# Kernel tuning notes

Measured on AMD Instinct MI355X. Metric: run time of the kernel, lower is better.

Reference implementation:

```python
import jax, jax.numpy as jnp
import numpy as np

B, N, M, H = 32, 1024, 128, 2  # batch, memory slots, word size, read heads
EPS = 1e-8


def setup_inputs() -> dict:
    key = jax.random.key(0)
    ks = jax.random.split(key, 6)
    return {
        "read_keys": jax.random.normal(ks[0], (B, H, M), jnp.float32),
        "read_strengths": jax.random.uniform(ks[1], (B, H), jnp.float32),
        "read_mode": jax.random.uniform(ks[2], (B, H, 3), jnp.float32),
        "W_old": jax.random.uniform(ks[3], (B, N), jnp.float32),
        "L": jax.random.uniform(ks[4], (B, N, N), jnp.float32),
        "memory": jax.random.normal(ks[5], (B, N, M), jnp.float32),
        "head_no": 0,
    }


def reference(read_keys, read_strengths, read_mode, W_old, L, memory, head_no):
    # Select this head's parameters
    k = read_keys[:, head_no, :]                      # [B, M]
    beta = read_strengths[:, head_no][:, None]        # [B, 1]
    rm = read_mode[:, head_no, :]                     # [B, 3] (backward, content, forward)

    # Temporal link transitions: f = L @ w_old, b = L^T @ w_old
    f = jnp.einsum('bij,bj->bi', L, W_old)            # [B, N]
    b = jnp.einsum('bji,bj->bi', L, W_old)            # [B, N]

    # Content-based addressing: softmax(beta * cosine_similarity(k, memory))
    sim = jnp.einsum('bnm,bm->bn', memory, k)         # [B, N]
    denom = (jnp.linalg.norm(memory, axis=-1)
             * jnp.linalg.norm(k, axis=-1, keepdims=True)) + EPS
    C = jax.nn.softmax(beta * sim / denom, axis=-1)   # [B, N]

    # Read-mode weighted combination
    W = rm[:, 0:1] * b + rm[:, 1:2] * C + rm[:, 2:3] * f  # [B, N]

    # Memory read
    mem_content = jnp.einsum('bn,bnm->bm', W, memory)     # [B, M]
    return (W, mem_content)
```

## Files before the change

### kernel.cpp

```cpp
#include <hip/hip_runtime.h>
#include <math.h>

#define EPS 1e-8f

constexpr int B = 32, N = 1024, M = 128, H = 2;

constexpr int ROWS_A   = 32;
constexpr int CHUNKS_A = N / ROWS_A;
constexpr int ROWS_C2   = 64;
constexpr int CHUNKS_C2 = N / ROWS_C2;

__global__ __launch_bounds__(256) void kA(const float* __restrict__ L,
                                          const float* __restrict__ Wold,
                                          float* __restrict__ f,
                                          float* __restrict__ bpart) {
    int bid   = blockIdx.x;
    int b     = bid / CHUNKS_A;
    int chunk = bid % CHUNKS_A;
    int t     = threadIdx.x;
    int lane  = t & 63, wave = t >> 6;

    __shared__ float sw[N];
    __shared__ float lds_b[4][N];

    reinterpret_cast<float4*>(sw)[t] =
        reinterpret_cast<const float4*>(Wold + (size_t)b * N)[t];
    __syncthreads();

    float4 wreg[4];
    float4 bacc[4];
#pragma unroll
    for (int s = 0; s < 4; ++s) {
        wreg[s] = reinterpret_cast<float4*>(sw)[lane + 64 * s];
        bacc[s] = make_float4(0.f, 0.f, 0.f, 0.f);
    }

    const float* Lb = L + (size_t)b * N * N;
    int r0 = chunk * ROWS_A;
    for (int r = wave; r < ROWS_A; r += 4) {
        int i = r0 + r;
        const float4* row = reinterpret_cast<const float4*>(Lb + (size_t)i * N);
        float wi = sw[i];
        float p  = 0.f;
#pragma unroll
        for (int s = 0; s < 4; ++s) {
            float4 v = row[lane + 64 * s];
            p += v.x * wreg[s].x + v.y * wreg[s].y + v.z * wreg[s].z + v.w * wreg[s].w;
            bacc[s].x += v.x * wi;
            bacc[s].y += v.y * wi;
            bacc[s].z += v.z * wi;
            bacc[s].w += v.w * wi;
        }
#pragma unroll
        for (int off = 32; off; off >>= 1) p += __shfl_down(p, off, 64);
        if (lane == 0) f[(size_t)b * N + i] = p;
    }

#pragma unroll
    for (int s = 0; s < 4; ++s)
        reinterpret_cast<float4*>(lds_b[wave])[lane + 64 * s] = bacc[s];
    __syncthreads();

    float4 s0 = reinterpret_cast<float4*>(lds_b[0])[t];
    float4 s1 = reinterpret_cast<float4*>(lds_b[1])[t];
    float4 s2 = reinterpret_cast<float4*>(lds_b[2])[t];
    float4 s3 = reinterpret_cast<float4*>(lds_b[3])[t];
    float4 o;
    o.x = s0.x + s1.x + s2.x + s3.x;
    o.y = s0.y + s1.y + s2.y + s3.y;
    o.z = s0.z + s1.z + s2.z + s3.z;
    o.w = s0.w + s1.w + s2.w + s3.w;
    reinterpret_cast<float4*>(bpart + ((size_t)b * CHUNKS_A + chunk) * N)[t] = o;
}

__global__ __launch_bounds__(256) void kB(const float* __restrict__ mem,
                                          const float* __restrict__ keys,
                                          const float* __restrict__ strengths,
                                          const int* __restrict__ head,
                                          float* __restrict__ logits) {
    int h    = head[0];
    int bid  = blockIdx.x;
    int b    = bid / (N / 4);
    int c    = bid % (N / 4);
    int lane = threadIdx.x & 63, wave = threadIdx.x >> 6;
    int n    = c * 4 + wave;

    float2 kv = reinterpret_cast<const float2*>(keys + ((size_t)b * H + h) * M)[lane];
    float2 mv = reinterpret_cast<const float2*>(mem + ((size_t)b * N + n) * M)[lane];

    float dot = mv.x * kv.x + mv.y * kv.y;
    float sm  = mv.x * mv.x + mv.y * mv.y;
    float sk  = kv.x * kv.x + kv.y * kv.y;
#pragma unroll
    for (int off = 32; off; off >>= 1) {
        dot += __shfl_down(dot, off, 64);
        sm  += __shfl_down(sm, off, 64);
        sk  += __shfl_down(sk, off, 64);
    }
    if (lane == 0) {
        float beta  = strengths[(size_t)b * H + h];
        float denom = sqrtf(sm) * sqrtf(sk) + EPS;
        logits[(size_t)b * N + n] = beta * dot / denom;
    }
}

__global__ __launch_bounds__(256) void kC1(const float* __restrict__ f,
                                           const float* __restrict__ bpart,
                                           const float* __restrict__ logits,
                                           const float* __restrict__ mode,
                                           const int* __restrict__ head,
                                           float* __restrict__ Wout) {
    int b = blockIdx.x;
    int t = threadIdx.x;
    int h = head[0];
    int lane = t & 63, wave = t >> 6;
    __shared__ float redmax[4];
    __shared__ float redsum[4];

    float lg[4], bs[4], fv[4];
    float mx = -1e30f;
#pragma unroll
    for (int q = 0; q < 4; ++q) {
        int n = t + 256 * q;
        lg[q] = logits[(size_t)b * N + n];
        fv[q] = f[(size_t)b * N + n];
        float s = 0.f;
        for (int c = 0; c < CHUNKS_A; ++c)
            s += bpart[((size_t)b * CHUNKS_A + c) * N + n];
        bs[q] = s;
        mx = fmaxf(mx, lg[q]);
    }
#pragma unroll
    for (int off = 32; off; off >>= 1) mx = fmaxf(mx, __shfl_down(mx, off, 64));
    if (lane == 0) redmax[wave] = mx;
    __syncthreads();
    mx = fmaxf(fmaxf(redmax[0], redmax[1]), fmaxf(redmax[2], redmax[3]));

    float ex[4];
    float se = 0.f;
#pragma unroll
    for (int q = 0; q < 4; ++q) { ex[q] = expf(lg[q] - mx); se += ex[q]; }
#pragma unroll
    for (int off = 32; off; off >>= 1) se += __shfl_down(se, off, 64);
    if (lane == 0) redsum[wave] = se;
    __syncthreads();
    se = redsum[0] + redsum[1] + redsum[2] + redsum[3];
    float inv = 1.f / se;

    const float* rm = mode + ((size_t)b * H + h) * 3;
    float rm0 = rm[0], rm1 = rm[1], rm2 = rm[2];
#pragma unroll
    for (int q = 0; q < 4; ++q) {
        int n = t + 256 * q;
        Wout[(size_t)b * N + n] = rm0 * bs[q] + rm1 * ex[q] * inv + rm2 * fv[q];
    }
}

__global__ __launch_bounds__(256) void kC2(const float* __restrict__ mem,
                                           const float* __restrict__ Wout,
                                           float* __restrict__ mcpart) {
    int bid   = blockIdx.x;
    int b     = bid / CHUNKS_C2;
    int chunk = bid % CHUNKS_C2;
    int t     = threadIdx.x;
    int cg    = t & 31;
    int rg    = t >> 5;
    __shared__ float4 lds[8][32];

    float4 acc = make_float4(0.f, 0.f, 0.f, 0.f);
    int r0 = chunk * ROWS_C2;
#pragma unroll
    for (int rr = 0; rr < ROWS_C2 / 8; ++rr) {
        int n   = r0 + rg + rr * 8;
        float w = Wout[(size_t)b * N + n];
        float4 v = reinterpret_cast<const float4*>(mem + ((size_t)b * N + n) * M)[cg];
        acc.x += w * v.x; acc.y += w * v.y; acc.z += w * v.z; acc.w += w * v.w;
    }
    lds[rg][cg] = acc;
    __syncthreads();
    if (t < 32) {
        float4 o = make_float4(0.f, 0.f, 0.f, 0.f);
#pragma unroll
        for (int g = 0; g < 8; ++g) {
            float4 v = lds[g][t];
            o.x += v.x; o.y += v.y; o.z += v.z; o.w += v.w;
        }
        reinterpret_cast<float4*>(mcpart + ((size_t)b * CHUNKS_C2 + chunk) * M)[t] = o;
    }
}

__global__ __launch_bounds__(256) void kC3(const float* __restrict__ mcpart,
                                           float* __restrict__ mc) {
    int idx = blockIdx.x * 256 + threadIdx.x;
    if (idx >= B * M) return;
    int b = idx / M, m = idx % M;
    float s = 0.f;
    for (int c = 0; c < CHUNKS_C2; ++c)
        s += mcpart[((size_t)b * CHUNKS_C2 + c) * M + m];
    mc[idx] = s;
}

extern "C" void kernel_launch(void* const* d_in, const int* in_sizes, int n_in,
                              void* d_out, int out_size, void* d_ws, size_t ws_size,
                              hipStream_t stream) {
    const float* read_keys      = (const float*)d_in[0];
    const float* read_strengths = (const float*)d_in[1];
    const float* read_mode      = (const float*)d_in[2];
    const float* W_old          = (const float*)d_in[3];
    const float* L              = (const float*)d_in[4];
    const float* memory         = (const float*)d_in[5];
    const int*   head_no        = (const int*)d_in[6];

    float* out_W  = (float*)d_out;
    float* out_mc = out_W + (size_t)B * N;

    float* ws     = (float*)d_ws;
    float* f      = ws;
    float* bpart  = f + (size_t)B * N;
    float* logits = bpart + (size_t)B * CHUNKS_A * N;
    float* mcpart = logits + (size_t)B * N;

    kA<<<B * CHUNKS_A, 256, 0, stream>>>(L, W_old, f, bpart);
    kB<<<B * (N / 4), 256, 0, stream>>>(memory, read_keys, read_strengths, head_no, logits);
    kC1<<<B, 256, 0, stream>>>(f, bpart, logits, read_mode, head_no, out_W);
    kC2<<<B * CHUNKS_C2, 256, 0, stream>>>(memory, out_W, mcpart);
    kC3<<<(B * M + 255) / 256, 256, 0, stream>>>(mcpart, out_mc);
}
```

Before: 44.07 us.

## Merge link and content kernels, split W into linear parts, cut launches to three

```diff
diff --git a/kernel.cpp b/kernel.cpp
--- a/kernel.cpp
+++ b/kernel.cpp
@@ -5,199 +5,223 @@
 
 constexpr int B = 32, N = 1024, M = 128, H = 2;
 
-constexpr int ROWS_A   = 32;
+constexpr int ROWS_A   = 16;
 constexpr int CHUNKS_A = N / ROWS_A;
-constexpr int ROWS_C2   = 64;
-constexpr int CHUNKS_C2 = N / ROWS_C2;
-
-__global__ __launch_bounds__(256) void kA(const float* __restrict__ L,
+constexpr int NBLK_A   = B * CHUNKS_A;
+constexpr int ROWS_B   = 64;
+constexpr int NBLK_B   = B * (N / ROWS_B);
+constexpr int ROWS_C   = 64;
+constexpr int CHUNKS_C = N / ROWS_C;
+
+__global__ __launch_bounds__(256) void k1(const float* __restrict__ L,
                                           const float* __restrict__ Wold,
-                                          float* __restrict__ f,
-                                          float* __restrict__ bpart) {
-    int bid   = blockIdx.x;
-    int b     = bid / CHUNKS_A;
-    int chunk = bid % CHUNKS_A;
-    int t     = threadIdx.x;
-    int lane  = t & 63, wave = t >> 6;
-
-    __shared__ float sw[N];
-    __shared__ float lds_b[4][N];
-
-    reinterpret_cast<float4*>(sw)[t] =
-        reinterpret_cast<const float4*>(Wold + (size_t)b * N)[t];
-    __syncthreads();
-
-    float4 wreg[4];
-    float4 bacc[4];
-#pragma unroll
-    for (int s = 0; s < 4; ++s) {
-        wreg[s] = reinterpret_cast<float4*>(sw)[lane + 64 * s];
-        bacc[s] = make_float4(0.f, 0.f, 0.f, 0.f);
-    }
-
-    const float* Lb = L + (size_t)b * N * N;
-    int r0 = chunk * ROWS_A;
-    for (int r = wave; r < ROWS_A; r += 4) {
-        int i = r0 + r;
-        const float4* row = reinterpret_cast<const float4*>(Lb + (size_t)i * N);
-        float wi = sw[i];
-        float p  = 0.f;
-#pragma unroll
-        for (int s = 0; s < 4; ++s) {
-            float4 v = row[lane + 64 * s];
-            p += v.x * wreg[s].x + v.y * wreg[s].y + v.z * wreg[s].z + v.w * wreg[s].w;
-            bacc[s].x += v.x * wi;
-            bacc[s].y += v.y * wi;
-            bacc[s].z += v.z * wi;
-            bacc[s].w += v.w * wi;
-        }
-#pragma unroll
-        for (int off = 32; off; off >>= 1) p += __shfl_down(p, off, 64);
-        if (lane == 0) f[(size_t)b * N + i] = p;
-    }
-
-#pragma unroll
-    for (int s = 0; s < 4; ++s)
-        reinterpret_cast<float4*>(lds_b[wave])[lane + 64 * s] = bacc[s];
-    __syncthreads();
-
-    float4 s0 = reinterpret_cast<float4*>(lds_b[0])[t];
-    float4 s1 = reinterpret_cast<float4*>(lds_b[1])[t];
-    float4 s2 = reinterpret_cast<float4*>(lds_b[2])[t];
-    float4 s3 = reinterpret_cast<float4*>(lds_b[3])[t];
-    float4 o;
-    o.x = s0.x + s1.x + s2.x + s3.x;
-    o.y = s0.y + s1.y + s2.y + s3.y;
-    o.z = s0.z + s1.z + s2.z + s3.z;
-    o.w = s0.w + s1.w + s2.w + s3.w;
-    reinterpret_cast<float4*>(bpart + ((size_t)b * CHUNKS_A + chunk) * N)[t] = o;
-}
-
-__global__ __launch_bounds__(256) void kB(const float* __restrict__ mem,
+                                          const float* __restrict__ mem,
                                           const float* __restrict__ keys,
                                           const float* __restrict__ strengths,
                                           const int* __restrict__ head,
-                                          float* __restrict__ logits) {
-    int h    = head[0];
+                                          float* __restrict__ f,
+                                          float* __restrict__ bpart,
+                                          float* __restrict__ e) {
     int bid  = blockIdx.x;
-    int b    = bid / (N / 4);
-    int c    = bid % (N / 4);
-    int lane = threadIdx.x & 63, wave = threadIdx.x >> 6;
-    int n    = c * 4 + wave;
-
-    float2 kv = reinterpret_cast<const float2*>(keys + ((size_t)b * H + h) * M)[lane];
-    float2 mv = reinterpret_cast<const float2*>(mem + ((size_t)b * N + n) * M)[lane];
-
-    float dot = mv.x * kv.x + mv.y * kv.y;
-    float sm  = mv.x * mv.x + mv.y * mv.y;
-    float sk  = kv.x * kv.x + kv.y * kv.y;
-#pragma unroll
-    for (int off = 32; off; off >>= 1) {
-        dot += __shfl_down(dot, off, 64);
-        sm  += __shfl_down(sm, off, 64);
-        sk  += __shfl_down(sk, off, 64);
-    }
-    if (lane == 0) {
-        float beta  = strengths[(size_t)b * H + h];
-        float denom = sqrtf(sm) * sqrtf(sk) + EPS;
-        logits[(size_t)b * N + n] = beta * dot / denom;
-    }
-}
-
-__global__ __launch_bounds__(256) void kC1(const float* __restrict__ f,
-                                           const float* __restrict__ bpart,
-                                           const float* __restrict__ logits,
-                                           const float* __restrict__ mode,
-                                           const int* __restrict__ head,
-                                           float* __restrict__ Wout) {
+    int t    = threadIdx.x;
+    int lane = t & 63, wave = t >> 6;
+
+    if (bid < NBLK_A) {
+        __shared__ float sw[N];
+        __shared__ float lds_b[4][N];
+
+        int b     = bid / CHUNKS_A;
+        int chunk = bid % CHUNKS_A;
+
+        reinterpret_cast<float4*>(sw)[t] =
+            reinterpret_cast<const float4*>(Wold + (size_t)b * N)[t];
+        __syncthreads();
+
+        float4 wreg[4];
+        float4 bacc[4];
+#pragma unroll
+        for (int s = 0; s < 4; ++s) {
+            wreg[s] = reinterpret_cast<float4*>(sw)[lane + 64 * s];
+            bacc[s] = make_float4(0.f, 0.f, 0.f, 0.f);
+        }
+
+        const float* Lb = L + (size_t)b * N * N;
+        int r0 = chunk * ROWS_A;
+        for (int r = wave; r < ROWS_A; r += 4) {
+            int i = r0 + r;
+            const float4* row = reinterpret_cast<const float4*>(Lb + (size_t)i * N);
+            float wi = sw[i];
+            float p  = 0.f;
+#pragma unroll
+            for (int s = 0; s < 4; ++s) {
+                float4 v = row[lane + 64 * s];
+                p += v.x * wreg[s].x + v.y * wreg[s].y + v.z * wreg[s].z + v.w * wreg[s].w;
+                bacc[s].x += v.x * wi;
+                bacc[s].y += v.y * wi;
+                bacc[s].z += v.z * wi;
+                bacc[s].w += v.w * wi;
+            }
+#pragma unroll
+            for (int off = 32; off; off >>= 1) p += __shfl_down(p, off, 64);
+            if (lane == 0) f[(size_t)b * N + i] = p;
+        }
+
+#pragma unroll
+        for (int s = 0; s < 4; ++s)
+            reinterpret_cast<float4*>(lds_b[wave])[lane + 64 * s] = bacc[s];
+        __syncthreads();
+
+        float4 s0 = reinterpret_cast<float4*>(lds_b[0])[t];
+        float4 s1 = reinterpret_cast<float4*>(lds_b[1])[t];
+        float4 s2 = reinterpret_cast<float4*>(lds_b[2])[t];
+        float4 s3 = reinterpret_cast<float4*>(lds_b[3])[t];
+        float4 o;
+        o.x = s0.x + s1.x + s2.x + s3.x;
+        o.y = s0.y + s1.y + s2.y + s3.y;
+        o.z = s0.z + s1.z + s2.z + s3.z;
+        o.w = s0.w + s1.w + s2.w + s3.w;
+        reinterpret_cast<float4*>(bpart + ((size_t)b * CHUNKS_A + chunk) * N)[t] = o;
+    } else {
+        int id    = bid - NBLK_A;
+        int b     = id / (N / ROWS_B);
+        int chunk = id % (N / ROWS_B);
+        int half  = lane >> 5;
+        int l32   = lane & 31;
+        int h     = head[0];
+
+        float4 kv = reinterpret_cast<const float4*>(keys + ((size_t)b * H + h) * M)[l32];
+        float  sk = kv.x * kv.x + kv.y * kv.y + kv.z * kv.z + kv.w * kv.w;
+#pragma unroll
+        for (int off = 16; off; off >>= 1) sk += __shfl_xor(sk, off, 64);
+        float norm_k = sqrtf(sk);
+        float beta   = strengths[(size_t)b * H + h];
+
+        int r0 = chunk * ROWS_B;
+#pragma unroll
+        for (int rr = 0; rr < ROWS_B / 8; ++rr) {
+            int n = r0 + rr * 8 + wave * 2 + half;
+            float4 mv = reinterpret_cast<const float4*>(mem + ((size_t)b * N + n) * M)[l32];
+            float dot = mv.x * kv.x + mv.y * kv.y + mv.z * kv.z + mv.w * kv.w;
+            float sm  = mv.x * mv.x + mv.y * mv.y + mv.z * mv.z + mv.w * mv.w;
+#pragma unroll
+            for (int off = 16; off; off >>= 1) {
+                dot += __shfl_xor(dot, off, 64);
+                sm  += __shfl_xor(sm, off, 64);
+            }
+            if (l32 == 0) {
+                float denom = sqrtf(sm) * norm_k + EPS;
+                e[(size_t)b * N + n] = expf(beta * dot / denom);
+            }
+        }
+    }
+}
+
+__global__ __launch_bounds__(256) void k2(const float* __restrict__ mem,
+                                          const float* __restrict__ bpart,
+                                          const float* __restrict__ f,
+                                          const float* __restrict__ e,
+                                          const float* __restrict__ mode,
+                                          const int* __restrict__ head,
+                                          float* __restrict__ U,
+                                          float* __restrict__ mcU,
+                                          float* __restrict__ mcE,
+                                          float* __restrict__ epart) {
+    int bid   = blockIdx.x;
+    int b     = bid / CHUNKS_C;
+    int chunk = bid % CHUNKS_C;
+    int t     = threadIdx.x;
+    int r0    = chunk * ROWS_C;
+
+    __shared__ float bp[4][ROWS_C];
+    __shared__ float su[ROWS_C], se[ROWS_C];
+    __shared__ float4 lU[8][32];
+    __shared__ float4 lE[8][32];
+
+    int n_ = t & 63, cg_ = t >> 6;
+    float s = 0.f;
+    for (int c = cg_; c < CHUNKS_A; c += 4)
+        s += bpart[((size_t)b * CHUNKS_A + c) * N + r0 + n_];
+    bp[cg_][n_] = s;
+    __syncthreads();
+
+    int h = head[0];
+    const float* rm = mode + ((size_t)b * H + h) * 3;
+    if (t < ROWS_C) {
+        float bsum = bp[0][t] + bp[1][t] + bp[2][t] + bp[3][t];
+        float u = rm[0] * bsum + rm[2] * f[(size_t)b * N + r0 + t];
+        su[t] = u;
+        U[(size_t)b * N + r0 + t] = u;
+        se[t] = e[(size_t)b * N + r0 + t];
+    }
+    __syncthreads();
+
+    int cg = t & 31, rg = t >> 5;
+    float4 aU = make_float4(0.f, 0.f, 0.f, 0.f);
+    float4 aE = make_float4(0.f, 0.f, 0.f, 0.f);
+#pragma unroll
+    for (int rr = 0; rr < ROWS_C / 8; ++rr) {
+        int r = rg + rr * 8;
+        float4 v = reinterpret_cast<const float4*>(mem + ((size_t)b * N + r0 + r) * M)[cg];
+        float uu = su[r], ee = se[r];
+        aU.x += uu * v.x; aU.y += uu * v.y; aU.z += uu * v.z; aU.w += uu * v.w;
+        aE.x += ee * v.x; aE.y += ee * v.y; aE.z += ee * v.z; aE.w += ee * v.w;
+    }
+    lU[rg][cg] = aU;
+    lE[rg][cg] = aE;
+    __syncthreads();
+
+    if (t < 32) {
+        float4 oU = make_float4(0.f, 0.f, 0.f, 0.f);
+        float4 oE = make_float4(0.f, 0.f, 0.f, 0.f);
+#pragma unroll
+        for (int g = 0; g < 8; ++g) {
+            float4 vU = lU[g][t], vE = lE[g][t];
+            oU.x += vU.x; oU.y += vU.y; oU.z += vU.z; oU.w += vU.w;
+            oE.x += vE.x; oE.y += vE.y; oE.z += vE.z; oE.w += vE.w;
+        }
+        reinterpret_cast<float4*>(mcU + ((size_t)b * CHUNKS_C + chunk) * M)[t] = oU;
+        reinterpret_cast<float4*>(mcE + ((size_t)b * CHUNKS_C + chunk) * M)[t] = oE;
+    } else if (t >= 64 && t < 128) {
+        float val = se[t - 64];
+#pragma unroll
+        for (int off = 32; off; off >>= 1) val += __shfl_down(val, off, 64);
+        if (t == 64) epart[(size_t)b * CHUNKS_C + chunk] = val;
+    }
+}
+
+__global__ __launch_bounds__(256) void k3(const float* __restrict__ U,
+                                          const float* __restrict__ e,
+                                          const float* __restrict__ mcU,
+                                          const float* __restrict__ mcE,
+                                          const float* __restrict__ epart,
+                                          const float* __restrict__ mode,
+                                          const int* __restrict__ head,
+                                          float* __restrict__ outW,
+                                          float* __restrict__ outMC) {
     int b = blockIdx.x;
     int t = threadIdx.x;
     int h = head[0];
-    int lane = t & 63, wave = t >> 6;
-    __shared__ float redmax[4];
-    __shared__ float redsum[4];
-
-    float lg[4], bs[4], fv[4];
-    float mx = -1e30f;
+    float rm1 = mode[((size_t)b * H + h) * 3 + 1];
+
+    float S = 0.f;
+#pragma unroll
+    for (int c = 0; c < CHUNKS_C; ++c) S += epart[(size_t)b * CHUNKS_C + c];
+    float coef = rm1 / S;
+
 #pragma unroll
     for (int q = 0; q < 4; ++q) {
         int n = t + 256 * q;
-        lg[q] = logits[(size_t)b * N + n];
-        fv[q] = f[(size_t)b * N + n];
-        float s = 0.f;
-        for (int c = 0; c < CHUNKS_A; ++c)
-            s += bpart[((size_t)b * CHUNKS_A + c) * N + n];
-        bs[q] = s;
-        mx = fmaxf(mx, lg[q]);
-    }
-#pragma unroll
-    for (int off = 32; off; off >>= 1) mx = fmaxf(mx, __shfl_down(mx, off, 64));
-    if (lane == 0) redmax[wave] = mx;
-    __syncthreads();
-    mx = fmaxf(fmaxf(redmax[0], redmax[1]), fmaxf(redmax[2], redmax[3]));
-
-    float ex[4];
-    float se = 0.f;
-#pragma unroll
-    for (int q = 0; q < 4; ++q) { ex[q] = expf(lg[q] - mx); se += ex[q]; }
-#pragma unroll
-    for (int off = 32; off; off >>= 1) se += __shfl_down(se, off, 64);
-    if (lane == 0) redsum[wave] = se;
-    __syncthreads();
-    se = redsum[0] + redsum[1] + redsum[2] + redsum[3];
-    float inv = 1.f / se;
-
-    const float* rm = mode + ((size_t)b * H + h) * 3;
-    float rm0 = rm[0], rm1 = rm[1], rm2 = rm[2];
-#pragma unroll
-    for (int q = 0; q < 4; ++q) {
-        int n = t + 256 * q;
-        Wout[(size_t)b * N + n] = rm0 * bs[q] + rm1 * ex[q] * inv + rm2 * fv[q];
-    }
-}
-
-__global__ __launch_bounds__(256) void kC2(const float* __restrict__ mem,
-                                           const float* __restrict__ Wout,
-                                           float* __restrict__ mcpart) {
-    int bid   = blockIdx.x;
-    int b     = bid / CHUNKS_C2;
-    int chunk = bid % CHUNKS_C2;
-    int t     = threadIdx.x;
-    int cg    = t & 31;
-    int rg    = t >> 5;
-    __shared__ float4 lds[8][32];
-
-    float4 acc = make_float4(0.f, 0.f, 0.f, 0.f);
-    int r0 = chunk * ROWS_C2;
-#pragma unroll
-    for (int rr = 0; rr < ROWS_C2 / 8; ++rr) {
-        int n   = r0 + rg + rr * 8;
-        float w = Wout[(size_t)b * N + n];
-        float4 v = reinterpret_cast<const float4*>(mem + ((size_t)b * N + n) * M)[cg];
-        acc.x += w * v.x; acc.y += w * v.y; acc.z += w * v.z; acc.w += w * v.w;
-    }
-    lds[rg][cg] = acc;
-    __syncthreads();
-    if (t < 32) {
-        float4 o = make_float4(0.f, 0.f, 0.f, 0.f);
-#pragma unroll
-        for (int g = 0; g < 8; ++g) {
-            float4 v = lds[g][t];
-            o.x += v.x; o.y += v.y; o.z += v.z; o.w += v.w;
-        }
-        reinterpret_cast<float4*>(mcpart + ((size_t)b * CHUNKS_C2 + chunk) * M)[t] = o;
-    }
-}
-
-__global__ __launch_bounds__(256) void kC3(const float* __restrict__ mcpart,
-                                           float* __restrict__ mc) {
-    int idx = blockIdx.x * 256 + threadIdx.x;
-    if (idx >= B * M) return;
-    int b = idx / M, m = idx % M;
-    float s = 0.f;
-    for (int c = 0; c < CHUNKS_C2; ++c)
-        s += mcpart[((size_t)b * CHUNKS_C2 + c) * M + m];
-    mc[idx] = s;
+        outW[(size_t)b * N + n] = U[(size_t)b * N + n] + coef * e[(size_t)b * N + n];
+    }
+    if (t < M) {
+        float sU = 0.f, sE = 0.f;
+#pragma unroll
+        for (int c = 0; c < CHUNKS_C; ++c) {
+            sU += mcU[((size_t)b * CHUNKS_C + c) * M + t];
+            sE += mcE[((size_t)b * CHUNKS_C + c) * M + t];
+        }
+        outMC[(size_t)b * M + t] = sU + coef * sE;
+    }
 }
 
 extern "C" void kernel_launch(void* const* d_in, const int* in_sizes, int n_in,
@@ -214,15 +238,19 @@
     float* out_W  = (float*)d_out;
     float* out_mc = out_W + (size_t)B * N;
 
-    float* ws     = (float*)d_ws;
-    float* f      = ws;
-    float* bpart  = f + (size_t)B * N;
-    float* logits = bpart + (size_t)B * CHUNKS_A * N;
-    float* mcpart = logits + (size_t)B * N;
-
-    kA<<<B * CHUNKS_A, 256, 0, stream>>>(L, W_old, f, bpart);
-    kB<<<B * (N / 4), 256, 0, stream>>>(memory, read_keys, read_strengths, head_no, logits);
-    kC1<<<B, 256, 0, stream>>>(f, bpart, logits, read_mode, head_no, out_W);
-    kC2<<<B * CHUNKS_C2, 256, 0, stream>>>(memory, out_W, mcpart);
-    kC3<<<(B * M + 255) / 256, 256, 0, stream>>>(mcpart, out_mc);
-}
+    float* ws    = (float*)d_ws;
+    float* f     = ws;
+    float* bpart = f + (size_t)B * N;
+    float* e     = bpart + (size_t)B * CHUNKS_A * N;
+    float* Ubuf  = e + (size_t)B * N;
+    float* mcU   = Ubuf + (size_t)B * N;
+    float* mcE   = mcU + (size_t)B * CHUNKS_C * M;
+    float* epart = mcE + (size_t)B * CHUNKS_C * M;
+
+    k1<<<NBLK_A + NBLK_B, 256, 0, stream>>>(L, W_old, memory, read_keys,
+                                            read_strengths, head_no, f, bpart, e);
+    k2<<<B * CHUNKS_C, 256, 0, stream>>>(memory, bpart, f, e, read_mode, head_no,
+                                         Ubuf, mcU, mcE, epart);
+    k3<<<B, 256, 0, stream>>>(Ubuf, e, mcU, mcE, epart, read_mode, head_no,
+                              out_W, out_mc);
+}
```

New measurement: 41.27 us. -6.4%, faster.
